# Kernel optimization log

Hardware: AMD Instinct MI355X
Metric: run time of the kernel (lower is better)

## Reference

```python
import jax, jax.numpy as jnp
import numpy as np

N_FULL, N_LOCAL, N_GLOBAL = 6, 4, 2
N_HEADS = N_FULL + N_LOCAL + N_GLOBAL
WINDOW = 64
DIM = 1536
B, S = 2, 2048


def setup_inputs() -> dict:
    key = jax.random.key(0)
    k0, k1, k2 = jax.random.split(key, 3)
    sc = DIM ** -0.5
    return {
        "x": jax.random.normal(k0, (B, S, DIM), dtype=jnp.float32),
        "Wqkv": jax.random.normal(k1, (DIM, 3 * DIM), dtype=jnp.float32) * sc,
        "bqkv": jnp.zeros((3 * DIM,), dtype=jnp.float32),
        "Wout": jax.random.normal(k2, (DIM, DIM), dtype=jnp.float32) * sc,
        "bout": jnp.zeros((DIM,), dtype=jnp.float32),
    }


def _attend(q, k, v, scale, bias=None):
    # q,k,v: [B,H,S,D]
    scores = jnp.einsum("bhqd,bhkd->bhqk", q, k) * scale
    if bias is not None:
        scores = scores + bias
    p = jax.nn.softmax(scores, axis=-1)
    return jnp.einsum("bhqk,bhkd->bhqd", p, v)


def reference(x, Wqkv, bqkv, Wout, bout):
    Bb, Ss, D = x.shape
    hd = D // N_HEADS
    scale = hd ** -0.5
    qkv = (x @ Wqkv + bqkv).reshape(Bb, Ss, 3, N_HEADS, hd)
    qkv = jnp.transpose(qkv, (2, 0, 3, 1, 4))  # [3,B,H,S,hd]
    q, k, v = qkv[0], qkv[1], qkv[2]
    h1 = N_FULL
    h2 = N_FULL + N_LOCAL

    # tier 1: full attention on first n_full heads
    out_full = _attend(q[:, :h1], k[:, :h1], v[:, :h1], scale)

    # tier 2: sliding-window (|i-j| <= window//2 allowed) on next n_local heads
    idx = jnp.arange(Ss)
    allowed = jnp.abs(idx[:, None] - idx[None, :]) <= WINDOW // 2  # [S,S]
    bias = jnp.where(allowed, 0.0, -jnp.inf).astype(x.dtype)[None, None]
    out_local = _attend(q[:, h1:h2], k[:, h1:h2], v[:, h1:h2], scale, bias)

    # tier 3: global — attend only to first and last tokens
    kg = jnp.stack([k[:, h2:, 0], k[:, h2:, -1]], axis=2)  # [B,Hg,2,hd]
    vg = jnp.stack([v[:, h2:, 0], v[:, h2:, -1]], axis=2)
    out_global = _attend(q[:, h2:], kg, vg, scale)

    out = jnp.concatenate([out_full, out_local, out_global], axis=1)  # [B,H,S,hd]
    out = jnp.transpose(out, (0, 2, 1, 3)).reshape(Bb, Ss, D)
    return out @ Wout + bout
```

## Files before the change

kernel.cpp:

```cpp
#include <hip/hip_runtime.h>
#include <hip/hip_bf16.h>

#define SEQ    2048
#define TOK    4096
#define DMODEL 1536
#define QKVROW 4608
#define HD     128
#define SCALE  0.08838834764831845f

#define NSPLIT 4
#define KRANGE (SEQ / NSPLIT)
#define NPAIR  12
#define ROWS_P (NPAIR * SEQ)
#define OPART_ELEMS ((size_t)ROWS_P * HD)

typedef __attribute__((ext_vector_type(8))) short short8;
typedef __attribute__((ext_vector_type(4))) short short4v;
typedef __attribute__((ext_vector_type(4))) float f32x4;

__device__ __forceinline__ float b2f(short s) {
    union { unsigned u; float f; } x;
    x.u = ((unsigned)(unsigned short)s) << 16;
    return x.f;
}
__device__ __forceinline__ short f2b(float f) {
    union { float f; unsigned u; } x; x.f = f;
    unsigned u = x.u;
    unsigned r = (u + 0x7fffu + ((u >> 16) & 1u)) >> 16;
    return (short)r;
}

__device__ __forceinline__ void gld_lds16(const short* g, short* l) {
    __builtin_amdgcn_global_load_lds(
        (__attribute__((address_space(1))) void*)(g),
        (__attribute__((address_space(3))) void*)(l), 16, 0, 0);
}

#define CVT_BLOCKS  6144
#define TQKV_BLOCKS 1728
#define TOUT_BLOCKS 576

__device__ __forceinline__ void transpose_tile(
    const float* __restrict__ W, short* __restrict__ WT,
    int K, int N, int k0, int n0, int t, short (*tile)[65])
{
    {
        int j  = t & 63;
        int i0 = (t >> 6) * 16;
        for (int ii = 0; ii < 16; ++ii)
            tile[i0 + ii][j] = f2b(W[(size_t)(k0 + i0 + ii) * N + n0 + j]);
    }
    __syncthreads();
    {
        int i  = t & 63;
        int j0 = (t >> 6) * 16;
        for (int jj = 0; jj < 16; ++jj)
            WT[(size_t)(n0 + j0 + jj) * K + k0 + i] = tile[i][j0 + jj];
    }
}

__global__ __launch_bounds__(256) void prepass_k(
    const float* __restrict__ x, const float* __restrict__ Wqkv,
    const float* __restrict__ Wout, short* __restrict__ xb,
    short* __restrict__ WqkvT, short* __restrict__ WoutT)
{
    __shared__ short tile[64][65];
    const int bid = blockIdx.x;
    const int t   = threadIdx.x;
    if (bid < CVT_BLOCKS) {
        int i = bid * 1024 + t * 4;
        float4 v = *(const float4*)(x + i);
        short4v b = { f2b(v.x), f2b(v.y), f2b(v.z), f2b(v.w) };
        *(short4v*)(xb + i) = b;
    } else if (bid < CVT_BLOCKS + TQKV_BLOCKS) {
        int tb = bid - CVT_BLOCKS;
        transpose_tile(Wqkv, WqkvT, DMODEL, QKVROW,
                       (tb / (QKVROW / 64)) * 64, (tb % (QKVROW / 64)) * 64, t, tile);
    } else {
        int tb = bid - (CVT_BLOCKS + TQKV_BLOCKS);
        transpose_tile(Wout, WoutT, DMODEL, DMODEL,
                       (tb / (DMODEL / 64)) * 64, (tb % (DMODEL / 64)) * 64, t, tile);
    }
}

__device__ __forceinline__ short* ldsP(short* base, int slot, int mat, int kh, int st) {
    return base + (((slot * 2 + mat) * 2 + kh) * 16 + st) * 512;
}

template <int SLOT, int KH, int G>
__device__ __forceinline__ void ld_a(short8 af[4], short* smem, int wm8, int lane) {
#pragma unroll
    for (int mi = 0; mi < 4; ++mi)
        af[mi] = *(const short8*)(ldsP(smem, SLOT, 0, KH, wm8 + G * 4 + mi) + lane * 8);
}
template <int SLOT, int KH>
__device__ __forceinline__ void ld_b(short8 bf[4], short* smem, int wn4, int lane) {
#pragma unroll
    for (int ni = 0; ni < 4; ++ni)
        bf[ni] = *(const short8*)(ldsP(smem, SLOT, 1, KH, wn4 + ni) + lane * 8);
}
template <int G>
__device__ __forceinline__ void mfma16(f32x4 (&acc)[8][4], const short8 af[4], const short8 bf[4]) {
#pragma unroll
    for (int mi = 0; mi < 4; ++mi)
#pragma unroll
        for (int ni = 0; ni < 4; ++ni)
            acc[G * 4 + mi][ni] = __builtin_amdgcn_mfma_f32_16x16x32_bf16(
                af[mi], bf[ni], acc[G * 4 + mi][ni], 0, 0, 0);
}

__device__ __forceinline__ void stage2(const short* g0, const short* g1, int ko,
                                       short* d0, short* d1) {
    gld_lds16(g0 + ko, d0);
    gld_lds16(g1 + ko, d1);
}

#define STG_A(S, KH, KT) stage2(gA0, gA1, (KT) * 64 + (KH) * 32, \
        ldsP(smem, (S), 0, (KH), wave), ldsP(smem, (S), 0, (KH), 8 + wave))
#define STG_B(S, KH, KT) stage2(gB0, gB1, (KT) * 64 + (KH) * 32, \
        ldsP(smem, (S), 1, (KH), wave), ldsP(smem, (S), 1, (KH), 8 + wave))

#define PH(S, KH, G, LOADB, STG_STMT, VMW)                          \
    do {                                                            \
        ld_a<S, KH, G>(af, smem, wm8, lane);                        \
        if (LOADB) ld_b<S, KH>(bf, smem, wn4, lane);                \
        STG_STMT;                                                   \
        asm volatile("" ::: "memory");                              \
        __builtin_amdgcn_s_barrier();                               \
        asm volatile("s_waitcnt lgkmcnt(0)" ::: "memory");          \
        __builtin_amdgcn_s_setprio(1);                              \
        mfma16<G>(acc, af, bf);                                     \
        __builtin_amdgcn_s_setprio(0);                              \
        if (VMW) asm volatile("s_waitcnt vmcnt(6)" ::: "memory");   \
        asm volatile("" ::: "memory");                              \
        __builtin_amdgcn_s_barrier();                               \
        asm volatile("" ::: "memory");                              \
    } while (0)

template <bool OUT_BF16>
__global__ __launch_bounds__(512, 2) void gemm256_8ph(
    const short* __restrict__ A, const short* __restrict__ BT,
    const float* __restrict__ bias, void* __restrict__ Cout,
    int N, int K)
{
    __shared__ short smem[2 * 2 * 2 * 16 * 512];

    const int t    = threadIdx.x;
    const int wave = t >> 6;
    const int lane = t & 63;
    const int quad = lane >> 4;
    const int lo   = lane & 15;
    const int wm   = wave >> 2;
    const int wn   = wave & 3;
    const int wm8  = wm * 8;
    const int wn4  = wn * 4;
    const int bn0  = blockIdx.x * 256;
    const int bm0  = blockIdx.y * 256;

    const int rO = quad * 8;
    const short* gA0 = A  + (size_t)(bm0 + wave * 16 + lo) * K + rO;
    const short* gA1 = A  + (size_t)(bm0 + (8 + wave) * 16 + lo) * K + rO;
    const short* gB0 = BT + (size_t)(bn0 + wave * 16 + lo) * K + rO;
    const short* gB1 = BT + (size_t)(bn0 + (8 + wave) * 16 + lo) * K + rO;

    f32x4 acc[8][4];
#pragma unroll
    for (int i = 0; i < 8; ++i)
#pragma unroll
        for (int j = 0; j < 4; ++j)
            acc[i][j] = (f32x4){0.f, 0.f, 0.f, 0.f};

    const int NT = K >> 6;

    STG_A(0, 0, 0); STG_A(0, 1, 0); STG_B(0, 0, 0); STG_B(0, 1, 0);
    STG_B(1, 0, 1); STG_A(1, 0, 1); STG_B(1, 1, 1);
    asm volatile("s_waitcnt vmcnt(6)" ::: "memory");
    asm volatile("" ::: "memory");
    __builtin_amdgcn_s_barrier();
    asm volatile("" ::: "memory");

    short8 af[4], bf[4];
#pragma unroll 1
    for (int it = 0; it < (NT >> 1); ++it) {
        const int T  = it * 2;
        const int t2 = min(T + 2, NT - 1);
        const int t3 = min(T + 3, NT - 1);
        PH(0, 0, 0, true,  STG_A(1, 1, T + 1), 0);
        PH(0, 0, 1, false, STG_B(0, 0, t2),    0);
        PH(0, 1, 0, true,  STG_A(0, 0, t2),    0);
        PH(0, 1, 1, false, STG_B(0, 1, t2),    1);
        PH(1, 0, 0, true,  STG_A(0, 1, t2),    0);
        PH(1, 0, 1, false, STG_B(1, 0, t3),    0);
        PH(1, 1, 0, true,  STG_A(1, 0, t3),    0);
        PH(1, 1, 1, false, STG_B(1, 1, t3),    1);
    }
    asm volatile("s_waitcnt vmcnt(0)" ::: "memory");

#pragma unroll
    for (int ni = 0; ni < 4; ++ni) {
        int col  = bn0 + wn * 64 + ni * 16 + lo;
        float bv = bias[col];
#pragma unroll
        for (int r8 = 0; r8 < 8; ++r8)
#pragma unroll
            for (int r = 0; r < 4; ++r) {
                int row   = bm0 + wm * 128 + r8 * 16 + quad * 4 + r;
                float val = acc[r8][ni][r] + bv;
                if (OUT_BF16)
                    ((short*)Cout)[(size_t)row * N + col] = f2b(val);
                else
                    ((float*)Cout)[(size_t)row * N + col] = val;
            }
    }
}

#define KSP 136
#define VTP 44
#define PLP 40

__global__ __launch_bounds__(256) void attn_full_split(
    const short* __restrict__ qkv, short* __restrict__ Opart,
    float* __restrict__ lsum)
{
    const int pair = blockIdx.y;
    const int b    = pair / 6;
    const int h    = pair % 6;
    const int q0   = blockIdx.x * 64;
    const int kz   = blockIdx.z;
    const int t    = threadIdx.x;
    const int wave = t >> 6;
    const int lane = t & 63;
    const int quad = lane >> 4;
    const int lo   = lane & 15;

    __shared__ short Ks[32 * KSP];
    __shared__ short Vr[32 * KSP];
    __shared__ short Vt[128 * VTP];
    __shared__ short Pl[4][16 * PLP];

    const short* base = qkv + (size_t)b * SEQ * QKVROW;

    short8 qf[4];
    {
        int qrow = q0 + wave * 16 + lo;
        const short* qp = base + (size_t)qrow * QKVROW + h * HD;
        for (int c = 0; c < 4; ++c)
            qf[c] = *(const short8*)(qp + c * 32 + quad * 8);
    }

    f32x4 o[8];
    for (int i = 0; i < 8; ++i) o[i] = (f32x4){0.f, 0.f, 0.f, 0.f};
    float lrow[4] = {0.f, 0.f, 0.f, 0.f};

    const int skey = t >> 3;
    const int sdc  = (t & 7) * 16;
    const int thd  = t & 127;
    const int tkc  = (t >> 7) * 16;

    const int kend = kz * KRANGE + KRANGE;
    for (int k0 = kz * KRANGE; k0 < kend; k0 += 32) {
        {
            const short* kro = base + (size_t)(k0 + skey) * QKVROW + DMODEL     + h * HD + sdc;
            const short* vro = base + (size_t)(k0 + skey) * QKVROW + 2 * DMODEL + h * HD + sdc;
            short8 ka = *(const short8*)kro;
            short8 kb = *(const short8*)(kro + 8);
            short8 va = *(const short8*)vro;
            short8 vb = *(const short8*)(vro + 8);
            *(short8*)(Ks + skey * KSP + sdc)     = ka;
            *(short8*)(Ks + skey * KSP + sdc + 8) = kb;
            *(short8*)(Vr + skey * KSP + sdc)     = va;
            *(short8*)(Vr + skey * KSP + sdc + 8) = vb;
        }
        __syncthreads();

        {
            short8 x0, x1;
            for (int j = 0; j < 8; ++j) x0[j] = Vr[(tkc + j) * KSP + thd];
            for (int j = 0; j < 8; ++j) x1[j] = Vr[(tkc + 8 + j) * KSP + thd];
            *(short8*)(Vt + thd * VTP + tkc)     = x0;
            *(short8*)(Vt + thd * VTP + tkc + 8) = x1;
        }

        f32x4 s[2];
        s[0] = (f32x4){0.f, 0.f, 0.f, 0.f};
        s[1] = (f32x4){0.f, 0.f, 0.f, 0.f};
        for (int g = 0; g < 2; ++g)
            for (int c = 0; c < 4; ++c) {
                short8 kf = *(const short8*)(Ks + (g * 16 + lo) * KSP + c * 32 + quad * 8);
                s[g] = __builtin_amdgcn_mfma_f32_16x16x32_bf16(qf[c], kf, s[g], 0, 0, 0);
            }

        for (int g = 0; g < 2; ++g)
            for (int r = 0; r < 4; ++r) {
                float p = __expf(s[g][r] * SCALE);
                lrow[r] += p;
                Pl[wave][(quad * 4 + r) * PLP + g * 16 + lo] = f2b(p);
            }
        __syncthreads();

        short8 pf = *(const short8*)(&Pl[wave][lo * PLP + quad * 8]);
        for (int ni = 0; ni < 8; ++ni) {
            short8 vf = *(const short8*)(Vt + (ni * 16 + lo) * VTP + quad * 8);
            o[ni] = __builtin_amdgcn_mfma_f32_16x16x32_bf16(pf, vf, o[ni], 0, 0, 0);
        }
    }

    for (int r = 0; r < 4; ++r)
        for (int off = 1; off < 16; off <<= 1)
            lrow[r] += __shfl_xor(lrow[r], off, 64);

    for (int ni = 0; ni < 8; ++ni)
        for (int r = 0; r < 4; ++r) {
            int grow = pair * SEQ + q0 + wave * 16 + quad * 4 + r;
            Opart[(size_t)kz * OPART_ELEMS + (size_t)grow * HD + ni * 16 + lo] =
                f2b(o[ni][r]);
        }
    if (lo == 0)
        for (int r = 0; r < 4; ++r) {
            int grow = pair * SEQ + q0 + wave * 16 + quad * 4 + r;
            lsum[kz * ROWS_P + grow] = lrow[r];
        }
}

__global__ __launch_bounds__(256) void attn_local_mfma(
    const short* __restrict__ qkv, short* __restrict__ att)
{
    const int pair = blockIdx.y;
    const int b    = pair >> 2;
    const int h    = 6 + (pair & 3);
    const int q0   = blockIdx.x * 64;
    const int t    = threadIdx.x;
    const int wave = t >> 6;
    const int lane = t & 63;
    const int quad = lane >> 4;
    const int lo   = lane & 15;

    __shared__ short Ks[32 * KSP];
    __shared__ short Vr[32 * KSP];
    __shared__ short Vt[128 * VTP];
    __shared__ short Pl[4][16 * PLP];

    const short* base = qkv + (size_t)b * SEQ * QKVROW;

    short8 qf[4];
    {
        int qrow = q0 + wave * 16 + lo;
        const short* qp = base + (size_t)qrow * QKVROW + h * HD;
        for (int c = 0; c < 4; ++c)
            qf[c] = *(const short8*)(qp + c * 32 + quad * 8);
    }

    f32x4 o[8];
    for (int i = 0; i < 8; ++i) o[i] = (f32x4){0.f, 0.f, 0.f, 0.f};
    float lrow[4] = {0.f, 0.f, 0.f, 0.f};

    const int skey = t >> 3;
    const int sdc  = (t & 7) * 16;
    const int thd  = t & 127;
    const int tkc  = (t >> 7) * 16;
    const int irow = q0 + wave * 16 + quad * 4;

    const int ks = max(0, q0 - 32);
    const int ke = min(SEQ, q0 + 96);
    for (int k0 = ks; k0 < ke; k0 += 32) {
        {
            const short* kro = base + (size_t)(k0 + skey) * QKVROW + DMODEL     + h * HD + sdc;
            const short* vro = base + (size_t)(k0 + skey) * QKVROW + 2 * DMODEL + h * HD + sdc;
            short8 ka = *(const short8*)kro;
            short8 kb = *(const short8*)(kro + 8);
            short8 va = *(const short8*)vro;
            short8 vb = *(const short8*)(vro + 8);
            *(short8*)(Ks + skey * KSP + sdc)     = ka;
            *(short8*)(Ks + skey * KSP + sdc + 8) = kb;
            *(short8*)(Vr + skey * KSP + sdc)     = va;
            *(short8*)(Vr + skey * KSP + sdc + 8) = vb;
        }
        __syncthreads();

        {
            short8 x0, x1;
            for (int j = 0; j < 8; ++j) x0[j] = Vr[(tkc + j) * KSP + thd];
            for (int j = 0; j < 8; ++j) x1[j] = Vr[(tkc + 8 + j) * KSP + thd];
            *(short8*)(Vt + thd * VTP + tkc)     = x0;
            *(short8*)(Vt + thd * VTP + tkc + 8) = x1;
        }

        f32x4 s[2];
        s[0] = (f32x4){0.f, 0.f, 0.f, 0.f};
        s[1] = (f32x4){0.f, 0.f, 0.f, 0.f};
        for (int g = 0; g < 2; ++g)
            for (int c = 0; c < 4; ++c) {
                short8 kf = *(const short8*)(Ks + (g * 16 + lo) * KSP + c * 32 + quad * 8);
                s[g] = __builtin_amdgcn_mfma_f32_16x16x32_bf16(qf[c], kf, s[g], 0, 0, 0);
            }

        for (int g = 0; g < 2; ++g)
            for (int r = 0; r < 4; ++r) {
                int j = k0 + g * 16 + lo;
                int d = irow + r - j;
                float p = (d >= -32 && d <= 32) ? __expf(s[g][r] * SCALE) : 0.f;
                lrow[r] += p;
                Pl[wave][(quad * 4 + r) * PLP + g * 16 + lo] = f2b(p);
            }
        __syncthreads();

        short8 pf = *(const short8*)(&Pl[wave][lo * PLP + quad * 8]);
        for (int ni = 0; ni < 8; ++ni) {
            short8 vf = *(const short8*)(Vt + (ni * 16 + lo) * VTP + quad * 8);
            o[ni] = __builtin_amdgcn_mfma_f32_16x16x32_bf16(pf, vf, o[ni], 0, 0, 0);
        }
    }

    for (int r = 0; r < 4; ++r)
        for (int off = 1; off < 16; off <<= 1)
            lrow[r] += __shfl_xor(lrow[r], off, 64);

    for (int ni = 0; ni < 8; ++ni)
        for (int r = 0; r < 4; ++r) {
            int row = irow + r;
            size_t off = ((size_t)(b * SEQ + row)) * DMODEL + h * HD + ni * 16 + lo;
            att[off] = f2b(o[ni][r] / lrow[r]);
        }
}

#define MERGE_BLOCKS  12288
#define GLOBAL_BLOCKS 2048

__global__ __launch_bounds__(256) void postattn_k(
    const short* __restrict__ qkv, const short* __restrict__ Opart,
    const float* __restrict__ lsum, short* __restrict__ att)
{
    const int bid  = blockIdx.x;
    const int t    = threadIdx.x;
    const int wave = t >> 6;
    const int lane = t & 63;

    if (bid < MERGE_BLOCKS) {
        int idx  = bid * 256 + t;
        int pair = idx >> 18;
        int q    = (idx >> 7) & (SEQ - 1);
        int hd   = idx & (HD - 1);
        int row  = pair * SEQ + q;
        float osum = 0.f, ls = 0.f;
        for (int z = 0; z < NSPLIT; ++z) {
            ls   += lsum[z * ROWS_P + row];
            osum += b2f(Opart[(size_t)z * OPART_ELEMS + (size_t)row * HD + hd]);
        }
        int b = pair / 6, h = pair % 6;
        att[((size_t)(b * SEQ + q)) * DMODEL + h * HD + hd] = f2b(osum / ls);
    } else {
        int gb   = bid - MERGE_BLOCKS;
        int pair = gb >> 9;
        int q    = (gb & 511) * 4 + wave;
        int b    = pair >> 1;
        int h    = 10 + (pair & 1);

        const short* base = qkv + (size_t)b * SEQ * QKVROW;
        const short* qp   = base + (size_t)q * QKVROW + h * HD;
        const short* k0   = base + DMODEL + h * HD;
        const short* k1   = base + (size_t)(SEQ - 1) * QKVROW + DMODEL + h * HD;

        float s0 = fmaf(b2f(qp[lane]), b2f(k0[lane]),
                   b2f(qp[lane + 64]) * b2f(k0[lane + 64]));
        float s1 = fmaf(b2f(qp[lane]), b2f(k1[lane]),
                   b2f(qp[lane + 64]) * b2f(k1[lane + 64]));
        for (int off = 1; off < 64; off <<= 1) {
            s0 += __shfl_xor(s0, off, 64);
            s1 += __shfl_xor(s1, off, 64);
        }
        s0 *= SCALE; s1 *= SCALE;
        float m  = fmaxf(s0, s1);
        float e0 = __expf(s0 - m), e1 = __expf(s1 - m);
        float inv = 1.f / (e0 + e1);
        float p0 = e0 * inv, p1 = e1 * inv;

        const short* v0 = base + 2 * DMODEL + h * HD;
        const short* v1 = base + (size_t)(SEQ - 1) * QKVROW + 2 * DMODEL + h * HD;
        size_t ob = ((size_t)(b * SEQ + q)) * DMODEL + h * HD;
        att[ob + lane]      = f2b(fmaf(p0, b2f(v0[lane]),      p1 * b2f(v1[lane])));
        att[ob + lane + 64] = f2b(fmaf(p0, b2f(v0[lane + 64]), p1 * b2f(v1[lane + 64])));
    }
}

extern "C" void kernel_launch(void* const* d_in, const int* in_sizes, int n_in,
                              void* d_out, int out_size, void* d_ws, size_t ws_size,
                              hipStream_t stream) {
    const float* x    = (const float*)d_in[0];
    const float* Wqkv = (const float*)d_in[1];
    const float* bqkv = (const float*)d_in[2];
    const float* Wout = (const float*)d_in[3];
    const float* bout = (const float*)d_in[4];

    char* p = (char*)d_ws;
    short* qkv   = (short*)p;  p += (size_t)TOK * QKVROW * 2;
    short* Opart = (short*)p;  p += OPART_ELEMS * NSPLIT * 2;
    float* lsum  = (float*)p;  p += (size_t)ROWS_P * NSPLIT * 4;
    short* xb    = (short*)p;  p += (size_t)TOK * DMODEL * 2;
    short* att   = xb;
    short* WqkvT = (short*)p;  p += (size_t)QKVROW * DMODEL * 2;
    short* WoutT = (short*)p;

    prepass_k<<<dim3(CVT_BLOCKS + TQKV_BLOCKS + TOUT_BLOCKS), 256, 0, stream>>>(
        x, Wqkv, Wout, xb, WqkvT, WoutT);
    gemm256_8ph<true><<<dim3(QKVROW / 256, TOK / 256), 512, 0, stream>>>(
        xb, WqkvT, bqkv, (void*)qkv, QKVROW, DMODEL);
    attn_full_split<<<dim3(SEQ / 64, NPAIR, NSPLIT), 256, 0, stream>>>(qkv, Opart, lsum);
    attn_local_mfma<<<dim3(SEQ / 64, 8), 256, 0, stream>>>(qkv, att);
    postattn_k<<<dim3(MERGE_BLOCKS + GLOBAL_BLOCKS), 256, 0, stream>>>(
        qkv, Opart, lsum, att);
    gemm256_8ph<false><<<dim3(DMODEL / 256, TOK / 256), 512, 0, stream>>>(
        att, WoutT, bout, d_out, DMODEL, DMODEL);
}
```

Measured before the change: 345.8 us.

## Shrink GEMM tiles to 128x256 and remap blocks for XCD-aware L2 locality

Measured after the change: 336.8 us. 1.03x faster.

```diff
diff --git a/kernel.cpp b/kernel.cpp
--- a/kernel.cpp
+++ b/kernel.cpp
@@ -83,67 +83,90 @@
     }
 }
 
-__device__ __forceinline__ short* ldsP(short* base, int slot, int mat, int kh, int st) {
-    return base + (((slot * 2 + mat) * 2 + kh) * 16 + st) * 512;
+__device__ __forceinline__ short* ldsA(short* s, int slot, int kh, int st) {
+    return s + ((slot * 2 + kh) * 8 + st) * 512;
+}
+__device__ __forceinline__ short* ldsB(short* s, int slot, int kh, int st) {
+    return s + 16384 + ((slot * 2 + kh) * 16 + st) * 512;
 }
 
 template <int SLOT, int KH, int G>
-__device__ __forceinline__ void ld_a(short8 af[4], short* smem, int wm8, int lane) {
-#pragma unroll
-    for (int mi = 0; mi < 4; ++mi)
-        af[mi] = *(const short8*)(ldsP(smem, SLOT, 0, KH, wm8 + G * 4 + mi) + lane * 8);
+__device__ __forceinline__ void ld_a(short8 af[2], short* smem, int wm4, int lane) {
+#pragma unroll
+    for (int mi = 0; mi < 2; ++mi)
+        af[mi] = *(const short8*)(ldsA(smem, SLOT, KH, wm4 + G * 2 + mi) + lane * 8);
 }
 template <int SLOT, int KH>
 __device__ __forceinline__ void ld_b(short8 bf[4], short* smem, int wn4, int lane) {
 #pragma unroll
     for (int ni = 0; ni < 4; ++ni)
-        bf[ni] = *(const short8*)(ldsP(smem, SLOT, 1, KH, wn4 + ni) + lane * 8);
+        bf[ni] = *(const short8*)(ldsB(smem, SLOT, KH, wn4 + ni) + lane * 8);
 }
 template <int G>
-__device__ __forceinline__ void mfma16(f32x4 (&acc)[8][4], const short8 af[4], const short8 bf[4]) {
-#pragma unroll
-    for (int mi = 0; mi < 4; ++mi)
+__device__ __forceinline__ void mfma8(f32x4 (&acc)[4][4], const short8 af[2], const short8 bf[4]) {
+#pragma unroll
+    for (int mi = 0; mi < 2; ++mi)
 #pragma unroll
         for (int ni = 0; ni < 4; ++ni)
-            acc[G * 4 + mi][ni] = __builtin_amdgcn_mfma_f32_16x16x32_bf16(
-                af[mi], bf[ni], acc[G * 4 + mi][ni], 0, 0, 0);
-}
-
-__device__ __forceinline__ void stage2(const short* g0, const short* g1, int ko,
-                                       short* d0, short* d1) {
-    gld_lds16(g0 + ko, d0);
-    gld_lds16(g1 + ko, d1);
-}
-
-#define STG_A(S, KH, KT) stage2(gA0, gA1, (KT) * 64 + (KH) * 32, \
-        ldsP(smem, (S), 0, (KH), wave), ldsP(smem, (S), 0, (KH), 8 + wave))
-#define STG_B(S, KH, KT) stage2(gB0, gB1, (KT) * 64 + (KH) * 32, \
-        ldsP(smem, (S), 1, (KH), wave), ldsP(smem, (S), 1, (KH), 8 + wave))
+            acc[G * 2 + mi][ni] = __builtin_amdgcn_mfma_f32_16x16x32_bf16(
+                af[mi], bf[ni], acc[G * 2 + mi][ni], 0, 0, 0);
+}
+
+#define STG_A(S, KH, KT) gld_lds16(gA0 + (KT) * 64 + (KH) * 32, ldsA(smem, (S), (KH), wave))
+#define STG_B(S, KH, KT)                                                        \
+    do {                                                                        \
+        gld_lds16(gB0 + (KT) * 64 + (KH) * 32, ldsB(smem, (S), (KH), wave));    \
+        gld_lds16(gB1 + (KT) * 64 + (KH) * 32, ldsB(smem, (S), (KH), 8 + wave));\
+    } while (0)
 
 #define PH(S, KH, G, LOADB, STG_STMT, VMW)                          \
     do {                                                            \
-        ld_a<S, KH, G>(af, smem, wm8, lane);                        \
+        ld_a<S, KH, G>(af, smem, wm4, lane);                        \
         if (LOADB) ld_b<S, KH>(bf, smem, wn4, lane);                \
         STG_STMT;                                                   \
         asm volatile("" ::: "memory");                              \
         __builtin_amdgcn_s_barrier();                               \
         asm volatile("s_waitcnt lgkmcnt(0)" ::: "memory");          \
         __builtin_amdgcn_s_setprio(1);                              \
-        mfma16<G>(acc, af, bf);                                     \
+        mfma8<G>(acc, af, bf);                                      \
         __builtin_amdgcn_s_setprio(0);                              \
-        if (VMW) asm volatile("s_waitcnt vmcnt(6)" ::: "memory");   \
+        if (VMW) asm volatile("s_waitcnt vmcnt(5)" ::: "memory");   \
         asm volatile("" ::: "memory");                              \
         __builtin_amdgcn_s_barrier();                               \
         asm volatile("" ::: "memory");                              \
     } while (0)
 
-template <bool OUT_BF16>
-__global__ __launch_bounds__(512, 2) void gemm256_8ph(
+template <bool OUT_BF16, int MT, int NT>
+__global__ __launch_bounds__(512, 2) void gemm128x256_8ph(
     const short* __restrict__ A, const short* __restrict__ BT,
     const float* __restrict__ bias, void* __restrict__ Cout,
     int N, int K)
 {
-    __shared__ short smem[2 * 2 * 2 * 16 * 512];
+    __shared__ short smem[49152];
+
+    constexpr int NWG = MT * NT;
+    constexpr int Q8  = NWG / 8, R8 = NWG % 8;
+    constexpr int BW  = 4;
+    constexpr int FULLB = NT / BW;
+    constexpr int TB  = FULLB * MT * BW;
+    constexpr int TW  = NT - FULLB * BW;
+    const int orig = blockIdx.x;
+    const int xcd  = orig & 7, idx = orig >> 3;
+    const int wg   = (xcd < R8 ? xcd * (Q8 + 1) : R8 * (Q8 + 1) + (xcd - R8) * Q8) + idx;
+    int mt, nt;
+    if (TW == 0 || wg < TB) {
+        int band = wg / (MT * BW);
+        int rem  = wg % (MT * BW);
+        mt = rem / BW;
+        nt = band * BW + rem % BW;
+    } else {
+        constexpr int TWD = TW ? TW : 1;
+        int rem = wg - TB;
+        mt = rem / TWD;
+        nt = FULLB * BW + rem % TWD;
+    }
+    const int bm0 = mt * 128;
+    const int bn0 = nt * 256;
 
     const int t    = threadIdx.x;
     const int wave = t >> 6;
@@ -152,39 +175,36 @@
     const int lo   = lane & 15;
     const int wm   = wave >> 2;
     const int wn   = wave & 3;
-    const int wm8  = wm * 8;
+    const int wm4  = wm * 4;
     const int wn4  = wn * 4;
-    const int bn0  = blockIdx.x * 256;
-    const int bm0  = blockIdx.y * 256;
 
     const int rO = quad * 8;
     const short* gA0 = A  + (size_t)(bm0 + wave * 16 + lo) * K + rO;
-    const short* gA1 = A  + (size_t)(bm0 + (8 + wave) * 16 + lo) * K + rO;
     const short* gB0 = BT + (size_t)(bn0 + wave * 16 + lo) * K + rO;
     const short* gB1 = BT + (size_t)(bn0 + (8 + wave) * 16 + lo) * K + rO;
 
-    f32x4 acc[8][4];
-#pragma unroll
-    for (int i = 0; i < 8; ++i)
+    f32x4 acc[4][4];
+#pragma unroll
+    for (int i = 0; i < 4; ++i)
 #pragma unroll
         for (int j = 0; j < 4; ++j)
             acc[i][j] = (f32x4){0.f, 0.f, 0.f, 0.f};
 
-    const int NT = K >> 6;
+    const int NTK = K >> 6;
 
     STG_A(0, 0, 0); STG_A(0, 1, 0); STG_B(0, 0, 0); STG_B(0, 1, 0);
     STG_B(1, 0, 1); STG_A(1, 0, 1); STG_B(1, 1, 1);
-    asm volatile("s_waitcnt vmcnt(6)" ::: "memory");
+    asm volatile("s_waitcnt vmcnt(5)" ::: "memory");
     asm volatile("" ::: "memory");
     __builtin_amdgcn_s_barrier();
     asm volatile("" ::: "memory");
 
-    short8 af[4], bf[4];
+    short8 af[2], bf[4];
 #pragma unroll 1
-    for (int it = 0; it < (NT >> 1); ++it) {
+    for (int it = 0; it < (NTK >> 1); ++it) {
         const int T  = it * 2;
-        const int t2 = min(T + 2, NT - 1);
-        const int t3 = min(T + 3, NT - 1);
+        const int t2 = min(T + 2, NTK - 1);
+        const int t3 = min(T + 3, NTK - 1);
         PH(0, 0, 0, true,  STG_A(1, 1, T + 1), 0);
         PH(0, 0, 1, false, STG_B(0, 0, t2),    0);
         PH(0, 1, 0, true,  STG_A(0, 0, t2),    0);
@@ -201,11 +221,11 @@
         int col  = bn0 + wn * 64 + ni * 16 + lo;
         float bv = bias[col];
 #pragma unroll
-        for (int r8 = 0; r8 < 8; ++r8)
+        for (int mi = 0; mi < 4; ++mi)
 #pragma unroll
             for (int r = 0; r < 4; ++r) {
-                int row   = bm0 + wm * 128 + r8 * 16 + quad * 4 + r;
-                float val = acc[r8][ni][r] + bv;
+                int row   = bm0 + wm * 64 + mi * 16 + quad * 4 + r;
+                float val = acc[mi][ni][r] + bv;
                 if (OUT_BF16)
                     ((short*)Cout)[(size_t)row * N + col] = f2b(val);
                 else
@@ -502,12 +522,12 @@
 
     prepass_k<<<dim3(CVT_BLOCKS + TQKV_BLOCKS + TOUT_BLOCKS), 256, 0, stream>>>(
         x, Wqkv, Wout, xb, WqkvT, WoutT);
-    gemm256_8ph<true><<<dim3(QKVROW / 256, TOK / 256), 512, 0, stream>>>(
+    gemm128x256_8ph<true, 32, 18><<<dim3(32 * 18), 512, 0, stream>>>(
         xb, WqkvT, bqkv, (void*)qkv, QKVROW, DMODEL);
     attn_full_split<<<dim3(SEQ / 64, NPAIR, NSPLIT), 256, 0, stream>>>(qkv, Opart, lsum);
     attn_local_mfma<<<dim3(SEQ / 64, 8), 256, 0, stream>>>(qkv, att);
     postattn_k<<<dim3(MERGE_BLOCKS + GLOBAL_BLOCKS), 256, 0, stream>>>(
         qkv, Opart, lsum, att);
-    gemm256_8ph<false><<<dim3(DMODEL / 256, TOK / 256), 512, 0, stream>>>(
+    gemm128x256_8ph<false, 32, 6><<<dim3(32 * 6), 512, 0, stream>>>(
         att, WoutT, bout, d_out, DMODEL, DMODEL);
 }
```
